# Kernel tuning notes

Measured on AMD Instinct MI355X. Metric: run time of the kernel, lower is better.

The kernel has to match this reference:

```python
import jax, jax.numpy as jnp
import numpy as np

EPS = 1e-5
CLUSTER_COUNT = 64
B, N, DV, DA = 128, 300, 1024, 128


def setup_inputs() -> dict:
    key = jax.random.key(0)
    k1, k2 = jax.random.split(key)
    video = jax.random.normal(k1, (B, N, DV), dtype=jnp.float32)
    audio = jax.random.normal(k2, (B, N, DA), dtype=jnp.float32)
    return {"video": video, "audio": audio}


def _select_indices(x_norm):
    """Greedy farthest-point (min |cosine|) selection for one batch. x_norm: [N, D]."""
    # indices starts as [0]; first appended index comes from sims of row 0
    best = jnp.abs(x_norm @ x_norm[0])          # [N]
    last = jnp.argmin(best)

    def step(carry, _):
        best, last = carry
        sims = jnp.abs(x_norm @ x_norm[last])   # [N]
        best = jnp.maximum(best, sims)
        new_last = jnp.argmin(best)
        return (best, new_last), new_last

    (_, _), rest = jax.lax.scan(step, (best, last), None, length=CLUSTER_COUNT - 2)
    idx = jnp.concatenate([jnp.array([0], dtype=last.dtype),
                           last[None], rest])  # [CLUSTER_COUNT]
    return jnp.sort(idx)


def reference(video, audio):
    # video: [B, N, DV], audio: [B, N, DA]
    norm = jnp.linalg.norm(video, axis=2) + EPS          # [B, N]
    video_normalized = video / norm[:, :, None]
    idx = jax.vmap(_select_indices)(video_normalized)     # [B, K], sorted
    v_sel = jnp.take_along_axis(video, idx[:, :, None], axis=1)  # [B, K, DV]
    a_sel = jnp.take_along_axis(audio, idx[:, :, None], axis=1)  # [B, K, DA]
    return v_sel, a_sel
```

## Files before the change

### kernel.cpp

```cpp
#include <hip/hip_runtime.h>
#include <math.h>


constexpr int BB = 128, NN = 300, DV = 1024, DA = 128, KK = 64;
constexpr int TRI = NN * (NN + 1) / 2;
constexpr int TB = 64;
constexpr int NTILES = 15;
constexpr int KC = 32;
constexpr int NCH = DV / KC;
constexpr int LDH = 36;

__device__ __constant__ int c_ib[NTILES] = {0,0,0,0,0, 1,1,1,1, 2,2,2, 3,3, 4};
__device__ __constant__ int c_jb[NTILES] = {0,1,2,3,4, 1,2,3,4, 2,3,4, 3,4, 4};

typedef _Float16 f16x8 __attribute__((ext_vector_type(8)));
typedef float    f32x4 __attribute__((ext_vector_type(4)));

union H4 { _Float16 h[4]; uint2 u; };
union F8 { uint2 u2[2]; f16x8 v; };

__device__ __forceinline__ int tri_base(int i) { return i * NN - (i * (i - 1)) / 2; }

__global__ __launch_bounds__(256) void kgram(const float* __restrict__ video,
                                             float* __restrict__ G) {
    const int bid  = blockIdx.x;
    const int swz  = (bid & 7) * 240 + (bid >> 3);
    const int batch = swz / 15;
    const int tile  = swz - batch * 15;
    const int i0 = c_ib[tile] * TB, j0 = c_jb[tile] * TB;
    const bool diag = (i0 == j0);
    const int tid = threadIdx.x;

    __shared__ _Float16 sH[2][4][TB][LDH];
    __shared__ float    s_part[256];
    __shared__ double   s_inv[2][TB];

    const float* vb = video + (size_t)batch * NN * DV;

    const int slab  = tid >> 7;
    const int lrow  = (tid >> 1) & 63;
    const int khalf = tid & 1;
    const int grow  = (slab ? j0 : i0) + lrow;
    const bool rok  = grow < NN;
    const bool stage_on = !(diag && slab == 1);
    const float4* srcb4 = (const float4*)(vb + (size_t)(rok ? grow : 0) * DV);
    const int qbase = khalf * 4;

    const int lane = tid & 63, w = tid >> 6;
    const int wr = w >> 1, wc = w & 1;
    const int g = lane >> 4, c16 = lane & 15;
    const int bplane = diag ? 0 : 2;

    f32x4 acc[2][2];
    #pragma unroll
    for (int fr = 0; fr < 2; ++fr)
        #pragma unroll
        for (int fc = 0; fc < 2; ++fc) acc[fr][fc] = (f32x4){0.f, 0.f, 0.f, 0.f};

    float ps = 0.f;
    float4 ld[4];
    const float4 z4 = make_float4(0.f, 0.f, 0.f, 0.f);

    auto stage_write = [&](int bf) {
        #pragma unroll
        for (int q = 0; q < 4; ++q) {
            float4 v = ld[q];
            ps = fmaf(v.x, v.x, fmaf(v.y, v.y, fmaf(v.z, v.z, fmaf(v.w, v.w, ps))));
            H4 hi, lo;
            _Float16 h0 = (_Float16)v.x, h1 = (_Float16)v.y,
                     h2 = (_Float16)v.z, h3 = (_Float16)v.w;
            hi.h[0] = h0; hi.h[1] = h1; hi.h[2] = h2; hi.h[3] = h3;
            lo.h[0] = (_Float16)(v.x - (float)h0);
            lo.h[1] = (_Float16)(v.y - (float)h1);
            lo.h[2] = (_Float16)(v.z - (float)h2);
            lo.h[3] = (_Float16)(v.w - (float)h3);
            const int p = khalf * 16 + 4 * q;
            *(uint2*)&sH[bf][slab * 2 + 0][lrow][p] = hi.u;
            *(uint2*)&sH[bf][slab * 2 + 1][lrow][p] = lo.u;
        }
    };

    if (stage_on) {
        #pragma unroll
        for (int q = 0; q < 4; ++q) ld[q] = rok ? srcb4[qbase + q] : z4;
        stage_write(0);
        #pragma unroll
        for (int q = 0; q < 4; ++q) ld[q] = rok ? srcb4[8 + qbase + q] : z4;
    }
    __syncthreads();

    for (int kc = 0; kc < NCH; ++kc) {
        const int cur = kc & 1, nxt = cur ^ 1;

        if (stage_on && kc < NCH - 1) stage_write(nxt);
        if (stage_on && kc < NCH - 2) {
            #pragma unroll
            for (int q = 0; q < 4; ++q)
                ld[q] = rok ? srcb4[(kc + 2) * 8 + qbase + q] : z4;
        }

        f16x8 Ah[2], Al[2], Bh[2], Bl[2];
        #pragma unroll
        for (int fr = 0; fr < 2; ++fr) {
            const int row = 32 * wr + 16 * fr + c16;
            F8 t;
            t.u2[0] = *(const uint2*)&sH[cur][0][row][4 * g];
            t.u2[1] = *(const uint2*)&sH[cur][0][row][16 + 4 * g];
            Ah[fr] = t.v;
            t.u2[0] = *(const uint2*)&sH[cur][1][row][4 * g];
            t.u2[1] = *(const uint2*)&sH[cur][1][row][16 + 4 * g];
            Al[fr] = t.v;
        }
        #pragma unroll
        for (int fc = 0; fc < 2; ++fc) {
            const int row = 32 * wc + 16 * fc + c16;
            F8 t;
            t.u2[0] = *(const uint2*)&sH[cur][bplane + 0][row][4 * g];
            t.u2[1] = *(const uint2*)&sH[cur][bplane + 0][row][16 + 4 * g];
            Bh[fc] = t.v;
            t.u2[0] = *(const uint2*)&sH[cur][bplane + 1][row][4 * g];
            t.u2[1] = *(const uint2*)&sH[cur][bplane + 1][row][16 + 4 * g];
            Bl[fc] = t.v;
        }
        #pragma unroll
        for (int fr = 0; fr < 2; ++fr)
            #pragma unroll
            for (int fc = 0; fc < 2; ++fc) {
                acc[fr][fc] = __builtin_amdgcn_mfma_f32_16x16x32_f16(Ah[fr], Bh[fc], acc[fr][fc], 0, 0, 0);
                acc[fr][fc] = __builtin_amdgcn_mfma_f32_16x16x32_f16(Ah[fr], Bl[fc], acc[fr][fc], 0, 0, 0);
                acc[fr][fc] = __builtin_amdgcn_mfma_f32_16x16x32_f16(Al[fr], Bh[fc], acc[fr][fc], 0, 0, 0);
            }

        __syncthreads();
    }

    s_part[tid] = ps;
    __syncthreads();
    if (tid < 128) {
        const int st = tid >> 6, r = tid & 63;
        const int src = (st && !diag) ? 128 + 2 * r : 2 * r;
        float ssum = s_part[src] + s_part[src + 1];
        s_inv[st][r] = 1.0 / (sqrt((double)ssum) + 1e-5);
    }
    __syncthreads();

    float* Gb = G + (size_t)batch * TRI;
    #pragma unroll
    for (int fr = 0; fr < 2; ++fr)
        #pragma unroll
        for (int fc = 0; fc < 2; ++fc)
            #pragma unroll
            for (int reg = 0; reg < 4; ++reg) {
                const int il = 32 * wr + 16 * fr + 4 * g + reg;
                const int jl = 32 * wc + 16 * fc + c16;
                const int i = i0 + il, j = j0 + jl;
                if (i <= j && j < NN)
                    Gb[tri_base(i) + (j - i)] =
                        (float)(fabs((double)acc[fr][fc][reg]) * s_inv[0][il] * s_inv[1][jl]);
            }
}

__device__ __forceinline__ void select_wave(const float* __restrict__ Gb,
                                            int lane, int* s_sorted) {
    float best[5];
    int myidx = 0;

    #pragma unroll
    for (int q = 0; q < 5; ++q) {
        int r = lane + 64 * q;
        best[q] = (r < NN) ? Gb[r] : 3.4e38f;
    }

    int last;
    {
        float v = INFINITY; int ri = 1 << 30;
        #pragma unroll
        for (int q = 0; q < 5; ++q)
            if (best[q] < v) { v = best[q]; ri = lane + 64 * q; }
        #pragma unroll
        for (int off = 32; off >= 1; off >>= 1) {
            float ov = __shfl_xor(v, off, 64); int oi = __shfl_xor(ri, off, 64);
            if (ov < v || (ov == v && oi < ri)) { v = ov; ri = oi; }
        }
        last = ri;
    }
    if (lane == 1) myidx = last;

    for (int t = 2; t < KK; ++t) {
        #pragma unroll
        for (int q = 0; q < 5; ++q) {
            int r = lane + 64 * q;
            if (r < NN) {
                int i = min(last, r), j = max(last, r);
                best[q] = fmaxf(best[q], Gb[tri_base(i) + (j - i)]);
            }
        }
        float v = INFINITY; int ri = 1 << 30;
        #pragma unroll
        for (int q = 0; q < 5; ++q)
            if (best[q] < v) { v = best[q]; ri = lane + 64 * q; }
        #pragma unroll
        for (int off = 32; off >= 1; off >>= 1) {
            float ov = __shfl_xor(v, off, 64); int oi = __shfl_xor(ri, off, 64);
            if (ov < v || (ov == v && oi < ri)) { v = ov; ri = oi; }
        }
        last = ri;
        if (lane == t) myidx = last;
    }

    int rank = 0;
    for (int j = 0; j < KK; ++j) {
        int oj = __shfl(myidx, j, 64);
        rank += (oj < myidx) || (oj == myidx && j < lane);
    }
    s_sorted[rank] = myidx;
}

__global__ __launch_bounds__(256) void kfused(const float* __restrict__ G,
                                              const float* __restrict__ video,
                                              const float* __restrict__ audio,
                                              float* __restrict__ out_v,
                                              float* __restrict__ out_a) {
    const int b = blockIdx.x, tid = threadIdx.x;
    __shared__ int s_sorted[KK];

    if (tid < 64)
        select_wave(G + (size_t)b * TRI, tid, s_sorted);
    __syncthreads();

    const float4* vb4 = (const float4*)(video + (size_t)b * NN * DV);
    float4* ov4 = (float4*)(out_v + (size_t)b * KK * DV);
    #pragma unroll 4
    for (int t = tid; t < KK * DV / 4; t += 256) {
        int k = t >> 8, c = t & 255;
        ov4[t] = vb4[s_sorted[k] * (DV / 4) + c];
    }
    const float4* ab4 = (const float4*)(audio + (size_t)b * NN * DA);
    float4* oa4 = (float4*)(out_a + (size_t)b * KK * DA);
    for (int t = tid; t < KK * DA / 4; t += 256) {
        int k = t >> 5, c = t & 31;
        oa4[t] = ab4[s_sorted[k] * (DA / 4) + c];
    }
}

__global__ __launch_bounds__(64) void kselect(const float* __restrict__ G,
                                              float* __restrict__ out_a) {
    __shared__ int s_sorted[KK];
    select_wave(G + (size_t)blockIdx.x * TRI, threadIdx.x, s_sorted);
    __syncthreads();
    ((int*)(out_a + (size_t)blockIdx.x * KK * DA))[threadIdx.x] = s_sorted[threadIdx.x];
}

__global__ __launch_bounds__(256) void kgather(const float* __restrict__ video,
                                               const float* __restrict__ audio,
                                               float* __restrict__ out_v,
                                               float* __restrict__ out_a) {
    int b = blockIdx.x, tid = threadIdx.x;
    __shared__ int s_idx[KK];
    const int* idxp = (const int*)(out_a + (size_t)b * KK * DA);
    if (tid < KK) s_idx[tid] = idxp[tid];
    __syncthreads();

    const float4* vb4 = (const float4*)(video + (size_t)b * NN * DV);
    float4* ov4 = (float4*)(out_v + (size_t)b * KK * DV);
    #pragma unroll 4
    for (int t = tid; t < KK * DV / 4; t += 256) {
        int k = t >> 8, c = t & 255;
        ov4[t] = vb4[s_idx[k] * (DV / 4) + c];
    }
    const float4* ab4 = (const float4*)(audio + (size_t)b * NN * DA);
    float4* oa4 = (float4*)(out_a + (size_t)b * KK * DA);
    for (int t = tid; t < KK * DA / 4; t += 256) {
        int k = t >> 5, c = t & 31;
        oa4[t] = ab4[s_idx[k] * (DA / 4) + c];
    }
}

extern "C" void kernel_launch(void* const* d_in, const int* in_sizes, int n_in,
                              void* d_out, int out_size, void* d_ws, size_t ws_size,
                              hipStream_t stream) {
    const float* video = (const float*)d_in[0];
    const float* audio = (const float*)d_in[1];
    float* out   = (float*)d_out;
    float* out_v = out;
    float* out_a = out + (size_t)BB * KK * DV;

    const size_t g_bytes = (size_t)BB * TRI * sizeof(float);
    if (ws_size >= g_bytes) {
        float* G = (float*)d_ws;
        kgram <<<NTILES * BB, 256, 0, stream>>>(video, G);
        kfused<<<BB, 256, 0, stream>>>(G, video, audio, out_v, out_a);
    } else {
        float* G = out;
        kgram  <<<NTILES * BB, 256, 0, stream>>>(video, G);
        kselect<<<BB, 64, 0, stream>>>(G, out_a);
        kgather<<<BB, 256, 0, stream>>>(video, audio, out_v, out_a);
    }
}
```

Baseline: 206.8 us.

## Pre-split video into fp16 hi/lo MFMA fragment layout before Gram kernel

Adds a prep kernel that converts each video row once into hi/lo fp16 pairs stored in the exact per-lane MFMA fragment order, and computes the inverse norms there. A new Gram kernel then loads fragments straight from global memory with no LDS staging or barriers. This removes the repeated fp32-to-fp16 split of the same rows across the five tiles that share them. The cost is an extra launch, a larger workspace, and an extra global write and read of the fragment buffer. The new path only runs when the workspace is big enough.

```diff
diff --git a/kernel.cpp b/kernel.cpp
--- a/kernel.cpp
+++ b/kernel.cpp
@@ -9,6 +9,14 @@
 constexpr int KC = 32;
 constexpr int NCH = DV / KC;
 constexpr int LDH = 36;
+constexpr int NRG = 20;
+
+constexpr size_t FRAG_U     = (size_t)NRG * NCH * 64;
+constexpr size_t FRAG_BYTES = FRAG_U * 16 * 2 * BB;
+constexpr size_t INV_OFF    = FRAG_BYTES;
+constexpr size_t INV_BYTES  = (size_t)BB * NN * 8;
+constexpr size_t G_OFF      = INV_OFF + INV_BYTES;
+constexpr size_t WS_NEED    = G_OFF + (size_t)BB * TRI * 4;
 
 __device__ __constant__ int c_ib[NTILES] = {0,0,0,0,0, 1,1,1,1, 2,2,2, 3,3, 4};
 __device__ __constant__ int c_jb[NTILES] = {0,1,2,3,4, 1,2,3,4, 2,3,4, 3,4, 4};
@@ -17,12 +25,128 @@
 typedef float    f32x4 __attribute__((ext_vector_type(4)));
 
 union H4 { _Float16 h[4]; uint2 u; };
+union H8 { _Float16 h[8]; f16x8 v; };
 union F8 { uint2 u2[2]; f16x8 v; };
 
 __device__ __forceinline__ int tri_base(int i) { return i * NN - (i * (i - 1)) / 2; }
 
-__global__ __launch_bounds__(256) void kgram(const float* __restrict__ video,
-                                             float* __restrict__ G) {
+__global__ __launch_bounds__(256) void kprep(const float* __restrict__ video,
+                                             _Float16* __restrict__ F,
+                                             double* __restrict__ invn) {
+    const int rg = blockIdx.x, b = blockIdx.y;
+    const int tid = threadIdx.x, w = tid >> 6, lane = tid & 63;
+    const int g = lane >> 4, c16 = lane & 15;
+    const int row = rg * 16 + c16;
+    const bool rv = row < NN;
+    const float* vr = video + (size_t)b * NN * DV + (size_t)(rv ? row : 0) * DV;
+    const float4 z4 = make_float4(0.f, 0.f, 0.f, 0.f);
+
+    f16x8* Fv = (f16x8*)F;
+    const size_t baseHi = ((size_t)(b * 2 + 0) * NRG + rg) * (NCH * 64) + lane;
+    const size_t baseLo = ((size_t)(b * 2 + 1) * NRG + rg) * (NCH * 64) + lane;
+
+    float ps = 0.f;
+    for (int kc = w; kc < NCH; kc += 4) {
+        const int k0 = kc * KC;
+        float4 a = rv ? *(const float4*)(vr + k0 + 4 * g) : z4;
+        float4 c = rv ? *(const float4*)(vr + k0 + 16 + 4 * g) : z4;
+        ps = fmaf(a.x, a.x, fmaf(a.y, a.y, fmaf(a.z, a.z, fmaf(a.w, a.w, ps))));
+        ps = fmaf(c.x, c.x, fmaf(c.y, c.y, fmaf(c.z, c.z, fmaf(c.w, c.w, ps))));
+        float s[8] = {a.x, a.y, a.z, a.w, c.x, c.y, c.z, c.w};
+        H8 hi, lo;
+        #pragma unroll
+        for (int e = 0; e < 8; ++e) {
+            _Float16 h = (_Float16)s[e];
+            hi.h[e] = h;
+            lo.h[e] = (_Float16)(s[e] - (float)h);
+        }
+        Fv[baseHi + kc * 64] = hi.v;
+        Fv[baseLo + kc * 64] = lo.v;
+    }
+
+    ps += __shfl_xor(ps, 16, 64);
+    ps += __shfl_xor(ps, 32, 64);
+    __shared__ float sr[4][16];
+    if (lane < 16) sr[w][c16] = ps;
+    __syncthreads();
+    if (tid < 16) {
+        const int rr = rg * 16 + tid;
+        if (rr < NN) {
+            double sum = (double)sr[0][tid] + (double)sr[1][tid]
+                       + (double)sr[2][tid] + (double)sr[3][tid];
+            invn[b * NN + rr] = 1.0 / (sqrt(sum) + 1e-5);
+        }
+    }
+}
+
+__global__ __launch_bounds__(256) void kgram2(const _Float16* __restrict__ F,
+                                              const double* __restrict__ invn,
+                                              float* __restrict__ G) {
+    const int bid  = blockIdx.x;
+    const int swz  = (bid & 7) * 240 + (bid >> 3);
+    const int batch = swz / 15;
+    const int tile  = swz - batch * 15;
+    const int i0 = c_ib[tile] * TB, j0 = c_jb[tile] * TB;
+    const int tid = threadIdx.x, lane = tid & 63, w = tid >> 6;
+    const int wr = w >> 1, wc = w & 1;
+    const int g = lane >> 4, c16 = lane & 15;
+
+    const f16x8* Fv = (const f16x8*)F;
+    const f16x8 *pAh[2], *pAl[2], *pBh[2], *pBl[2];
+    #pragma unroll
+    for (int fr = 0; fr < 2; ++fr) {
+        const int rgA = (i0 >> 4) + 2 * wr + fr;
+        const int rgB = (j0 >> 4) + 2 * wc + fr;
+        pAh[fr] = Fv + ((size_t)(batch * 2 + 0) * NRG + rgA) * (NCH * 64) + lane;
+        pAl[fr] = Fv + ((size_t)(batch * 2 + 1) * NRG + rgA) * (NCH * 64) + lane;
+        pBh[fr] = Fv + ((size_t)(batch * 2 + 0) * NRG + rgB) * (NCH * 64) + lane;
+        pBl[fr] = Fv + ((size_t)(batch * 2 + 1) * NRG + rgB) * (NCH * 64) + lane;
+    }
+
+    f32x4 acc[2][2];
+    #pragma unroll
+    for (int fr = 0; fr < 2; ++fr)
+        #pragma unroll
+        for (int fc = 0; fc < 2; ++fc) acc[fr][fc] = (f32x4){0.f, 0.f, 0.f, 0.f};
+
+    #pragma unroll 2
+    for (int kc = 0; kc < NCH; ++kc) {
+        const int o = kc * 64;
+        f16x8 Ah[2], Al[2], Bh[2], Bl[2];
+        #pragma unroll
+        for (int fr = 0; fr < 2; ++fr) {
+            Ah[fr] = pAh[fr][o]; Al[fr] = pAl[fr][o];
+            Bh[fr] = pBh[fr][o]; Bl[fr] = pBl[fr][o];
+        }
+        #pragma unroll
+        for (int fr = 0; fr < 2; ++fr)
+            #pragma unroll
+            for (int fc = 0; fc < 2; ++fc) {
+                acc[fr][fc] = __builtin_amdgcn_mfma_f32_16x16x32_f16(Ah[fr], Bh[fc], acc[fr][fc], 0, 0, 0);
+                acc[fr][fc] = __builtin_amdgcn_mfma_f32_16x16x32_f16(Ah[fr], Bl[fc], acc[fr][fc], 0, 0, 0);
+                acc[fr][fc] = __builtin_amdgcn_mfma_f32_16x16x32_f16(Al[fr], Bh[fc], acc[fr][fc], 0, 0, 0);
+            }
+    }
+
+    const double* invb = invn + batch * NN;
+    float* Gb = G + (size_t)batch * TRI;
+    #pragma unroll
+    for (int fr = 0; fr < 2; ++fr)
+        #pragma unroll
+        for (int fc = 0; fc < 2; ++fc)
+            #pragma unroll
+            for (int reg = 0; reg < 4; ++reg) {
+                const int il = 32 * wr + 16 * fr + 4 * g + reg;
+                const int jl = 32 * wc + 16 * fc + c16;
+                const int i = i0 + il, j = j0 + jl;
+                if (i <= j && j < NN)
+                    Gb[tri_base(i) + (j - i)] =
+                        (float)(fabs((double)acc[fr][fc][reg]) * invb[i] * invb[j]);
+            }
+}
+
+__global__ __launch_bounds__(256) void kgram_lds(const float* __restrict__ video,
+                                                 float* __restrict__ G) {
     const int bid  = blockIdx.x;
     const int swz  = (bid & 7) * 240 + (bid >> 3);
     const int batch = swz / 15;
@@ -91,7 +215,6 @@
 
     for (int kc = 0; kc < NCH; ++kc) {
         const int cur = kc & 1, nxt = cur ^ 1;
-
         if (stage_on && kc < NCH - 1) stage_write(nxt);
         if (stage_on && kc < NCH - 2) {
             #pragma unroll
@@ -130,7 +253,6 @@
                 acc[fr][fc] = __builtin_amdgcn_mfma_f32_16x16x32_f16(Ah[fr], Bl[fc], acc[fr][fc], 0, 0, 0);
                 acc[fr][fc] = __builtin_amdgcn_mfma_f32_16x16x32_f16(Al[fr], Bh[fc], acc[fr][fc], 0, 0, 0);
             }
-
         __syncthreads();
     }
 
@@ -286,14 +408,22 @@
     float* out_a = out + (size_t)BB * KK * DV;
 
     const size_t g_bytes = (size_t)BB * TRI * sizeof(float);
-    if (ws_size >= g_bytes) {
+
+    if (ws_size >= WS_NEED) {
+        _Float16* F  = (_Float16*)d_ws;
+        double* invn = (double*)((char*)d_ws + INV_OFF);
+        float* G     = (float*)((char*)d_ws + G_OFF);
+        kprep <<<dim3(NRG, BB), 256, 0, stream>>>(video, F, invn);
+        kgram2<<<NTILES * BB, 256, 0, stream>>>(F, invn, G);
+        kfused<<<BB, 256, 0, stream>>>(G, video, audio, out_v, out_a);
+    } else if (ws_size >= g_bytes) {
         float* G = (float*)d_ws;
-        kgram <<<NTILES * BB, 256, 0, stream>>>(video, G);
-        kfused<<<BB, 256, 0, stream>>>(G, video, audio, out_v, out_a);
+        kgram_lds<<<NTILES * BB, 256, 0, stream>>>(video, G);
+        kfused   <<<BB, 256, 0, stream>>>(G, video, audio, out_v, out_a);
     } else {
         float* G = out;
-        kgram  <<<NTILES * BB, 256, 0, stream>>>(video, G);
-        kselect<<<BB, 64, 0, stream>>>(G, out_a);
-        kgather<<<BB, 256, 0, stream>>>(video, audio, out_v, out_a);
-    }
-}
+        kgram_lds<<<NTILES * BB, 256, 0, stream>>>(video, G);
+        kselect  <<<BB, 64, 0, stream>>>(G, out_a);
+        kgather  <<<BB, 256, 0, stream>>>(video, audio, out_v, out_a);
+    }
+}
```

Result: slower. 272.8 us (+31.9%).

## Use 128x128 gram tiles and a padded square gram matrix for selection

Applied to the files above, without the earlier changes.

Adds a new gram kernel that uses 512-thread blocks computing 128x128 tiles, six per batch instead of fifteen 64x64 tiles. This gives more operand reuse per LDS load and fewer redundant video reads. The kernel writes the gram matrix as a full symmetric square with a padded stride of 304, so the selection loop reads a contiguous row instead of the triangular layout. The cost is a larger workspace, twice as many global stores, and higher register pressure from the larger accumulator. The older triangular path remains as a fallback when the workspace is too small.

```diff
diff --git a/kernel.cpp b/kernel.cpp
--- a/kernel.cpp
+++ b/kernel.cpp
@@ -4,12 +4,20 @@
 
 constexpr int BB = 128, NN = 300, DV = 1024, DA = 128, KK = 64;
 constexpr int TRI = NN * (NN + 1) / 2;
-constexpr int TB = 64;
-constexpr int NTILES = 15;
 constexpr int KC = 32;
 constexpr int NCH = DV / KC;
 constexpr int LDH = 36;
 
+constexpr int GS = 304;
+constexpr int GBATCH = NN * GS;
+constexpr size_t SQ_NEED = (size_t)BB * GBATCH * 4;
+
+constexpr int NT2 = 6;
+__device__ __constant__ int t2_ib[NT2] = {0,0,0,1,1,2};
+__device__ __constant__ int t2_jb[NT2] = {0,1,2,1,2,2};
+
+constexpr int NTILES = 15;
+constexpr int TB = 64;
 __device__ __constant__ int c_ib[NTILES] = {0,0,0,0,0, 1,1,1,1, 2,2,2, 3,3, 4};
 __device__ __constant__ int c_jb[NTILES] = {0,1,2,3,4, 1,2,3,4, 2,3,4, 3,4, 4};
 
@@ -21,25 +29,26 @@
 
 __device__ __forceinline__ int tri_base(int i) { return i * NN - (i * (i - 1)) / 2; }
 
-__global__ __launch_bounds__(256) void kgram(const float* __restrict__ video,
-                                             float* __restrict__ G) {
+__global__ __launch_bounds__(512, 4) void kgram3(const float* __restrict__ video,
+                                                 float* __restrict__ G) {
     const int bid  = blockIdx.x;
-    const int swz  = (bid & 7) * 240 + (bid >> 3);
-    const int batch = swz / 15;
-    const int tile  = swz - batch * 15;
-    const int i0 = c_ib[tile] * TB, j0 = c_jb[tile] * TB;
+    const int swz  = (bid & 7) * 96 + (bid >> 3);
+    const int batch = swz / NT2;
+    const int tile  = swz - batch * NT2;
+    const int i0 = t2_ib[tile] * 128, j0 = t2_jb[tile] * 128;
     const bool diag = (i0 == j0);
     const int tid = threadIdx.x;
 
-    __shared__ _Float16 sH[2][4][TB][LDH];
-    __shared__ float    s_part[256];
-    __shared__ double   s_inv[2][TB];
+    __shared__ _Float16 sH[2][4][128][LDH];
+    __shared__ float    s_part[512];
+    __shared__ double   s_inv[2][128];
 
     const float* vb = video + (size_t)batch * NN * DV;
 
-    const int slab  = tid >> 7;
-    const int lrow  = (tid >> 1) & 63;
-    const int khalf = tid & 1;
+    const int slab  = tid >> 8;
+    const int st    = tid & 255;
+    const int lrow  = st >> 1;
+    const int khalf = st & 1;
     const int grow  = (slab ? j0 : i0) + lrow;
     const bool rok  = grow < NN;
     const bool stage_on = !(diag && slab == 1);
@@ -47,13 +56,13 @@
     const int qbase = khalf * 4;
 
     const int lane = tid & 63, w = tid >> 6;
-    const int wr = w >> 1, wc = w & 1;
+    const int wr2 = w >> 2, wc2 = w & 3;
     const int g = lane >> 4, c16 = lane & 15;
     const int bplane = diag ? 0 : 2;
 
-    f32x4 acc[2][2];
+    f32x4 acc[4][2];
     #pragma unroll
-    for (int fr = 0; fr < 2; ++fr)
+    for (int fr = 0; fr < 4; ++fr)
         #pragma unroll
         for (int fc = 0; fc < 2; ++fc) acc[fr][fc] = (f32x4){0.f, 0.f, 0.f, 0.f};
 
@@ -91,7 +100,146 @@
 
     for (int kc = 0; kc < NCH; ++kc) {
         const int cur = kc & 1, nxt = cur ^ 1;
-
+        if (stage_on && kc < NCH - 1) stage_write(nxt);
+        if (stage_on && kc < NCH - 2) {
+            #pragma unroll
+            for (int q = 0; q < 4; ++q)
+                ld[q] = rok ? srcb4[(kc + 2) * 8 + qbase + q] : z4;
+        }
+
+        f16x8 Ah[4], Al[4], Bh[2], Bl[2];
+        #pragma unroll
+        for (int fr = 0; fr < 4; ++fr) {
+            const int row = 64 * wr2 + 16 * fr + c16;
+            F8 t;
+            t.u2[0] = *(const uint2*)&sH[cur][0][row][4 * g];
+            t.u2[1] = *(const uint2*)&sH[cur][0][row][16 + 4 * g];
+            Ah[fr] = t.v;
+            t.u2[0] = *(const uint2*)&sH[cur][1][row][4 * g];
+            t.u2[1] = *(const uint2*)&sH[cur][1][row][16 + 4 * g];
+            Al[fr] = t.v;
+        }
+        #pragma unroll
+        for (int fc = 0; fc < 2; ++fc) {
+            const int row = 32 * wc2 + 16 * fc + c16;
+            F8 t;
+            t.u2[0] = *(const uint2*)&sH[cur][bplane + 0][row][4 * g];
+            t.u2[1] = *(const uint2*)&sH[cur][bplane + 0][row][16 + 4 * g];
+            Bh[fc] = t.v;
+            t.u2[0] = *(const uint2*)&sH[cur][bplane + 1][row][4 * g];
+            t.u2[1] = *(const uint2*)&sH[cur][bplane + 1][row][16 + 4 * g];
+            Bl[fc] = t.v;
+        }
+        #pragma unroll
+        for (int fr = 0; fr < 4; ++fr)
+            #pragma unroll
+            for (int fc = 0; fc < 2; ++fc) {
+                acc[fr][fc] = __builtin_amdgcn_mfma_f32_16x16x32_f16(Ah[fr], Bh[fc], acc[fr][fc], 0, 0, 0);
+                acc[fr][fc] = __builtin_amdgcn_mfma_f32_16x16x32_f16(Ah[fr], Bl[fc], acc[fr][fc], 0, 0, 0);
+                acc[fr][fc] = __builtin_amdgcn_mfma_f32_16x16x32_f16(Al[fr], Bh[fc], acc[fr][fc], 0, 0, 0);
+            }
+        __syncthreads();
+    }
+
+    s_part[tid] = ps;
+    __syncthreads();
+    if (tid < 256) {
+        const int sl = tid >> 7, r = tid & 127;
+        const int src = (sl && !diag) ? 256 + 2 * r : 2 * r;
+        float ssum = s_part[src] + s_part[src + 1];
+        s_inv[sl][r] = 1.0 / (sqrt((double)ssum) + 1e-5);
+    }
+    __syncthreads();
+
+    float* Gb = G + (size_t)batch * GBATCH;
+    #pragma unroll
+    for (int fr = 0; fr < 4; ++fr)
+        #pragma unroll
+        for (int fc = 0; fc < 2; ++fc)
+            #pragma unroll
+            for (int reg = 0; reg < 4; ++reg) {
+                const int il = 64 * wr2 + 16 * fr + 4 * g + reg;
+                const int jl = 32 * wc2 + 16 * fc + c16;
+                const int i = i0 + il, j = j0 + jl;
+                if (i <= j && j < NN) {
+                    float val = (float)(fabs((double)acc[fr][fc][reg]) *
+                                        s_inv[0][il] * s_inv[1][jl]);
+                    Gb[i * GS + j] = val;
+                    Gb[j * GS + i] = val;
+                }
+            }
+}
+
+__global__ __launch_bounds__(256) void kgram_lds(const float* __restrict__ video,
+                                                 float* __restrict__ G) {
+    const int bid  = blockIdx.x;
+    const int swz  = (bid & 7) * 240 + (bid >> 3);
+    const int batch = swz / 15;
+    const int tile  = swz - batch * 15;
+    const int i0 = c_ib[tile] * TB, j0 = c_jb[tile] * TB;
+    const bool diag = (i0 == j0);
+    const int tid = threadIdx.x;
+
+    __shared__ _Float16 sH[2][4][TB][LDH];
+    __shared__ float    s_part[256];
+    __shared__ double   s_inv[2][TB];
+
+    const float* vb = video + (size_t)batch * NN * DV;
+
+    const int slab  = tid >> 7;
+    const int lrow  = (tid >> 1) & 63;
+    const int khalf = tid & 1;
+    const int grow  = (slab ? j0 : i0) + lrow;
+    const bool rok  = grow < NN;
+    const bool stage_on = !(diag && slab == 1);
+    const float4* srcb4 = (const float4*)(vb + (size_t)(rok ? grow : 0) * DV);
+    const int qbase = khalf * 4;
+
+    const int lane = tid & 63, w = tid >> 6;
+    const int wr = w >> 1, wc = w & 1;
+    const int g = lane >> 4, c16 = lane & 15;
+    const int bplane = diag ? 0 : 2;
+
+    f32x4 acc[2][2];
+    #pragma unroll
+    for (int fr = 0; fr < 2; ++fr)
+        #pragma unroll
+        for (int fc = 0; fc < 2; ++fc) acc[fr][fc] = (f32x4){0.f, 0.f, 0.f, 0.f};
+
+    float ps = 0.f;
+    float4 ld[4];
+    const float4 z4 = make_float4(0.f, 0.f, 0.f, 0.f);
+
+    auto stage_write = [&](int bf) {
+        #pragma unroll
+        for (int q = 0; q < 4; ++q) {
+            float4 v = ld[q];
+            ps = fmaf(v.x, v.x, fmaf(v.y, v.y, fmaf(v.z, v.z, fmaf(v.w, v.w, ps))));
+            H4 hi, lo;
+            _Float16 h0 = (_Float16)v.x, h1 = (_Float16)v.y,
+                     h2 = (_Float16)v.z, h3 = (_Float16)v.w;
+            hi.h[0] = h0; hi.h[1] = h1; hi.h[2] = h2; hi.h[3] = h3;
+            lo.h[0] = (_Float16)(v.x - (float)h0);
+            lo.h[1] = (_Float16)(v.y - (float)h1);
+            lo.h[2] = (_Float16)(v.z - (float)h2);
+            lo.h[3] = (_Float16)(v.w - (float)h3);
+            const int p = khalf * 16 + 4 * q;
+            *(uint2*)&sH[bf][slab * 2 + 0][lrow][p] = hi.u;
+            *(uint2*)&sH[bf][slab * 2 + 1][lrow][p] = lo.u;
+        }
+    };
+
+    if (stage_on) {
+        #pragma unroll
+        for (int q = 0; q < 4; ++q) ld[q] = rok ? srcb4[qbase + q] : z4;
+        stage_write(0);
+        #pragma unroll
+        for (int q = 0; q < 4; ++q) ld[q] = rok ? srcb4[8 + qbase + q] : z4;
+    }
+    __syncthreads();
+
+    for (int kc = 0; kc < NCH; ++kc) {
+        const int cur = kc & 1, nxt = cur ^ 1;
         if (stage_on && kc < NCH - 1) stage_write(nxt);
         if (stage_on && kc < NCH - 2) {
             #pragma unroll
@@ -130,17 +278,16 @@
                 acc[fr][fc] = __builtin_amdgcn_mfma_f32_16x16x32_f16(Ah[fr], Bl[fc], acc[fr][fc], 0, 0, 0);
                 acc[fr][fc] = __builtin_amdgcn_mfma_f32_16x16x32_f16(Al[fr], Bh[fc], acc[fr][fc], 0, 0, 0);
             }
-
         __syncthreads();
     }
 
     s_part[tid] = ps;
     __syncthreads();
     if (tid < 128) {
-        const int st = tid >> 6, r = tid & 63;
-        const int src = (st && !diag) ? 128 + 2 * r : 2 * r;
+        const int sl = tid >> 6, r = tid & 63;
+        const int src = (sl && !diag) ? 128 + 2 * r : 2 * r;
         float ssum = s_part[src] + s_part[src + 1];
-        s_inv[st][r] = 1.0 / (sqrt((double)ssum) + 1e-5);
+        s_inv[sl][r] = 1.0 / (sqrt((double)ssum) + 1e-5);
     }
     __syncthreads();
 
@@ -160,8 +307,62 @@
             }
 }
 
-__device__ __forceinline__ void select_wave(const float* __restrict__ Gb,
-                                            int lane, int* s_sorted) {
+__device__ __forceinline__ void select_wave_sq(const float* __restrict__ Gb,
+                                               int lane, int* s_sorted) {
+    float best[5];
+    int myidx = 0;
+
+    #pragma unroll
+    for (int q = 0; q < 5; ++q) {
+        int r = lane + 64 * q;
+        best[q] = (r < NN) ? Gb[r] : 3.4e38f;
+    }
+
+    int last;
+    {
+        float v = INFINITY; int ri = 1 << 30;
+        #pragma unroll
+        for (int q = 0; q < 5; ++q)
+            if (best[q] < v) { v = best[q]; ri = lane + 64 * q; }
+        #pragma unroll
+        for (int off = 32; off >= 1; off >>= 1) {
+            float ov = __shfl_xor(v, off, 64); int oi = __shfl_xor(ri, off, 64);
+            if (ov < v || (ov == v && oi < ri)) { v = ov; ri = oi; }
+        }
+        last = ri;
+    }
+    if (lane == 1) myidx = last;
+
+    for (int t = 2; t < KK; ++t) {
+        const float* row = Gb + last * GS;
+        #pragma unroll
+        for (int q = 0; q < 5; ++q) {
+            int r = lane + 64 * q;
+            if (r < NN) best[q] = fmaxf(best[q], row[r]);
+        }
+        float v = INFINITY; int ri = 1 << 30;
+        #pragma unroll
+        for (int q = 0; q < 5; ++q)
+            if (best[q] < v) { v = best[q]; ri = lane + 64 * q; }
+        #pragma unroll
+        for (int off = 32; off >= 1; off >>= 1) {
+            float ov = __shfl_xor(v, off, 64); int oi = __shfl_xor(ri, off, 64);
+            if (ov < v || (ov == v && oi < ri)) { v = ov; ri = oi; }
+        }
+        last = ri;
+        if (lane == t) myidx = last;
+    }
+
+    int rank = 0;
+    for (int j = 0; j < KK; ++j) {
+        int oj = __shfl(myidx, j, 64);
+        rank += (oj < myidx) || (oj == myidx && j < lane);
+    }
+    s_sorted[rank] = myidx;
+}
+
+__device__ __forceinline__ void select_wave_tri(const float* __restrict__ Gb,
+                                                int lane, int* s_sorted) {
     float best[5];
     int myidx = 0;
 
@@ -216,16 +417,16 @@
     s_sorted[rank] = myidx;
 }
 
-__global__ __launch_bounds__(256) void kfused(const float* __restrict__ G,
-                                              const float* __restrict__ video,
-                                              const float* __restrict__ audio,
-                                              float* __restrict__ out_v,
-                                              float* __restrict__ out_a) {
+__global__ __launch_bounds__(256) void kfused_sq(const float* __restrict__ G,
+                                                 const float* __restrict__ video,
+                                                 const float* __restrict__ audio,
+                                                 float* __restrict__ out_v,
+                                                 float* __restrict__ out_a) {
     const int b = blockIdx.x, tid = threadIdx.x;
     __shared__ int s_sorted[KK];
 
     if (tid < 64)
-        select_wave(G + (size_t)b * TRI, tid, s_sorted);
+        select_wave_sq(G + (size_t)b * GBATCH, tid, s_sorted);
     __syncthreads();
 
     const float4* vb4 = (const float4*)(video + (size_t)b * NN * DV);
@@ -243,10 +444,37 @@
     }
 }
 
+__global__ __launch_bounds__(256) void kfused_tri(const float* __restrict__ G,
+                                                  const float* __restrict__ video,
+                                                  const float* __restrict__ audio,
+                                                  float* __restrict__ out_v,
+                                                  float* __restrict__ out_a) {
+    const int b = blockIdx.x, tid = threadIdx.x;
+    __shared__ int s_sorted[KK];
+
+    if (tid < 64)
+        select_wave_tri(G + (size_t)b * TRI, tid, s_sorted);
+    __syncthreads();
+
+    const float4* vb4 = (const float4*)(video + (size_t)b * NN * DV);
+    float4* ov4 = (float4*)(out_v + (size_t)b * KK * DV);
+    #pragma unroll 4
+    for (int t = tid; t < KK * DV / 4; t += 256) {
+        int k = t >> 8, c = t & 255;
+        ov4[t] = vb4[s_sorted[k] * (DV / 4) + c];
+    }
+    const float4* ab4 = (const float4*)(audio + (size_t)b * NN * DA);
+    float4* oa4 = (float4*)(out_a + (size_t)b * KK * DA);
+    for (int t = tid; t < KK * DA / 4; t += 256) {
+        int k = t >> 5, c = t & 31;
+        oa4[t] = ab4[s_sorted[k] * (DA / 4) + c];
+    }
+}
+
 __global__ __launch_bounds__(64) void kselect(const float* __restrict__ G,
                                               float* __restrict__ out_a) {
     __shared__ int s_sorted[KK];
-    select_wave(G + (size_t)blockIdx.x * TRI, threadIdx.x, s_sorted);
+    select_wave_tri(G + (size_t)blockIdx.x * TRI, threadIdx.x, s_sorted);
     __syncthreads();
     ((int*)(out_a + (size_t)blockIdx.x * KK * DA))[threadIdx.x] = s_sorted[threadIdx.x];
 }
@@ -285,15 +513,20 @@
     float* out_v = out;
     float* out_a = out + (size_t)BB * KK * DV;
 
-    const size_t g_bytes = (size_t)BB * TRI * sizeof(float);
-    if (ws_size >= g_bytes) {
+    const size_t tri_bytes = (size_t)BB * TRI * sizeof(float);
+
+    if (ws_size >= SQ_NEED) {
         float* G = (float*)d_ws;
-        kgram <<<NTILES * BB, 256, 0, stream>>>(video, G);
-        kfused<<<BB, 256, 0, stream>>>(G, video, audio, out_v, out_a);
+        kgram3   <<<NT2 * BB, 512, 0, stream>>>(video, G);
+        kfused_sq<<<BB, 256, 0, stream>>>(G, video, audio, out_v, out_a);
+    } else if (ws_size >= tri_bytes) {
+        float* G = (float*)d_ws;
+        kgram_lds <<<NTILES * BB, 256, 0, stream>>>(video, G);
+        kfused_tri<<<BB, 256, 0, stream>>>(G, video, audio, out_v, out_a);
     } else {
         float* G = out;
-        kgram  <<<NTILES * BB, 256, 0, stream>>>(video, G);
-        kselect<<<BB, 64, 0, stream>>>(G, out_a);
-        kgather<<<BB, 256, 0, stream>>>(video, audio, out_v, out_a);
-    }
-}
+        kgram_lds<<<NTILES * BB, 256, 0, stream>>>(video, G);
+        kselect  <<<BB, 64, 0, stream>>>(G, out_a);
+        kgather  <<<BB, 256, 0, stream>>>(video, audio, out_v, out_a);
+    }
+}
```

Measured after the change: 214.6 us. +3.7%, slower.

## Use 512-thread gram blocks, pad per-batch triangle, and prefetch G in select kernel

Applied to the files above, without the earlier changes.

The gram kernel now runs 8 waves per block, so each wave computes a 32x16 sub-tile and each thread stages two float4 loads per chunk instead of four. This is meant to raise parallelism and hide latency. The per-batch triangle stride is padded to a 16-byte aligned size so the fused kernel can sweep the whole batch's G slab with float4 loads first. That sweep warms the cache before the serial greedy selection wave reads it. The cost is extra global reads and a dummy reduction, and each loaded B fragment is now reused by fewer MFMAs.

```diff
diff --git a/kernel.cpp b/kernel.cpp
--- a/kernel.cpp
+++ b/kernel.cpp
@@ -3,7 +3,8 @@
 
 
 constexpr int BB = 128, NN = 300, DV = 1024, DA = 128, KK = 64;
-constexpr int TRI = NN * (NN + 1) / 2;
+constexpr int TRI  = NN * (NN + 1) / 2;
+constexpr int TRIP = 45152;
 constexpr int TB = 64;
 constexpr int NTILES = 15;
 constexpr int KC = 32;
@@ -21,8 +22,8 @@
 
 __device__ __forceinline__ int tri_base(int i) { return i * NN - (i * (i - 1)) / 2; }
 
-__global__ __launch_bounds__(256) void kgram(const float* __restrict__ video,
-                                             float* __restrict__ G) {
+__global__ __launch_bounds__(512) void kgram512(const float* __restrict__ video,
+                                                float* __restrict__ G) {
     const int bid  = blockIdx.x;
     const int swz  = (bid & 7) * 240 + (bid >> 3);
     const int batch = swz / 15;
@@ -32,38 +33,37 @@
     const int tid = threadIdx.x;
 
     __shared__ _Float16 sH[2][4][TB][LDH];
-    __shared__ float    s_part[256];
+    __shared__ float    s_part[512];
     __shared__ double   s_inv[2][TB];
 
     const float* vb = video + (size_t)batch * NN * DV;
 
-    const int slab  = tid >> 7;
-    const int lrow  = (tid >> 1) & 63;
-    const int khalf = tid & 1;
-    const int grow  = (slab ? j0 : i0) + lrow;
-    const bool rok  = grow < NN;
+    const int slab = tid >> 8;
+    const int st   = tid & 255;
+    const int lrow = st >> 2;
+    const int part = st & 3;
+    const int grow = (slab ? j0 : i0) + lrow;
+    const bool rok = grow < NN;
     const bool stage_on = !(diag && slab == 1);
     const float4* srcb4 = (const float4*)(vb + (size_t)(rok ? grow : 0) * DV);
-    const int qbase = khalf * 4;
+    const int qbase = part * 2;
 
     const int lane = tid & 63, w = tid >> 6;
-    const int wr = w >> 1, wc = w & 1;
+    const int wr3 = w >> 2, wc3 = w & 3;
     const int g = lane >> 4, c16 = lane & 15;
     const int bplane = diag ? 0 : 2;
 
-    f32x4 acc[2][2];
-    #pragma unroll
-    for (int fr = 0; fr < 2; ++fr)
-        #pragma unroll
-        for (int fc = 0; fc < 2; ++fc) acc[fr][fc] = (f32x4){0.f, 0.f, 0.f, 0.f};
+    f32x4 acc[2];
+    acc[0] = (f32x4){0.f, 0.f, 0.f, 0.f};
+    acc[1] = (f32x4){0.f, 0.f, 0.f, 0.f};
 
     float ps = 0.f;
-    float4 ld[4];
+    float4 ld[2];
     const float4 z4 = make_float4(0.f, 0.f, 0.f, 0.f);
 
     auto stage_write = [&](int bf) {
         #pragma unroll
-        for (int q = 0; q < 4; ++q) {
+        for (int q = 0; q < 2; ++q) {
             float4 v = ld[q];
             ps = fmaf(v.x, v.x, fmaf(v.y, v.y, fmaf(v.z, v.z, fmaf(v.w, v.w, ps))));
             H4 hi, lo;
@@ -74,18 +74,18 @@
             lo.h[1] = (_Float16)(v.y - (float)h1);
             lo.h[2] = (_Float16)(v.z - (float)h2);
             lo.h[3] = (_Float16)(v.w - (float)h3);
-            const int p = khalf * 16 + 4 * q;
+            const int p = part * 8 + 4 * q;
             *(uint2*)&sH[bf][slab * 2 + 0][lrow][p] = hi.u;
             *(uint2*)&sH[bf][slab * 2 + 1][lrow][p] = lo.u;
         }
     };
 
     if (stage_on) {
-        #pragma unroll
-        for (int q = 0; q < 4; ++q) ld[q] = rok ? srcb4[qbase + q] : z4;
+        ld[0] = rok ? srcb4[qbase] : z4;
+        ld[1] = rok ? srcb4[qbase + 1] : z4;
         stage_write(0);
-        #pragma unroll
-        for (int q = 0; q < 4; ++q) ld[q] = rok ? srcb4[8 + qbase + q] : z4;
+        ld[0] = rok ? srcb4[8 + qbase] : z4;
+        ld[1] = rok ? srcb4[8 + qbase + 1] : z4;
     }
     __syncthreads();
 
@@ -94,15 +94,14 @@
 
         if (stage_on && kc < NCH - 1) stage_write(nxt);
         if (stage_on && kc < NCH - 2) {
-            #pragma unroll
-            for (int q = 0; q < 4; ++q)
-                ld[q] = rok ? srcb4[(kc + 2) * 8 + qbase + q] : z4;
-        }
-
-        f16x8 Ah[2], Al[2], Bh[2], Bl[2];
+            ld[0] = rok ? srcb4[(kc + 2) * 8 + qbase] : z4;
+            ld[1] = rok ? srcb4[(kc + 2) * 8 + qbase + 1] : z4;
+        }
+
+        f16x8 Ah[2], Al[2], Bh, Bl;
         #pragma unroll
         for (int fr = 0; fr < 2; ++fr) {
-            const int row = 32 * wr + 16 * fr + c16;
+            const int row = 32 * wr3 + 16 * fr + c16;
             F8 t;
             t.u2[0] = *(const uint2*)&sH[cur][0][row][4 * g];
             t.u2[1] = *(const uint2*)&sH[cur][0][row][16 + 4 * g];
@@ -111,25 +110,22 @@
             t.u2[1] = *(const uint2*)&sH[cur][1][row][16 + 4 * g];
             Al[fr] = t.v;
         }
-        #pragma unroll
-        for (int fc = 0; fc < 2; ++fc) {
-            const int row = 32 * wc + 16 * fc + c16;
+        {
+            const int row = 16 * wc3 + c16;
             F8 t;
             t.u2[0] = *(const uint2*)&sH[cur][bplane + 0][row][4 * g];
             t.u2[1] = *(const uint2*)&sH[cur][bplane + 0][row][16 + 4 * g];
-            Bh[fc] = t.v;
+            Bh = t.v;
             t.u2[0] = *(const uint2*)&sH[cur][bplane + 1][row][4 * g];
             t.u2[1] = *(const uint2*)&sH[cur][bplane + 1][row][16 + 4 * g];
-            Bl[fc] = t.v;
-        }
-        #pragma unroll
-        for (int fr = 0; fr < 2; ++fr)
-            #pragma unroll
-            for (int fc = 0; fc < 2; ++fc) {
-                acc[fr][fc] = __builtin_amdgcn_mfma_f32_16x16x32_f16(Ah[fr], Bh[fc], acc[fr][fc], 0, 0, 0);
-                acc[fr][fc] = __builtin_amdgcn_mfma_f32_16x16x32_f16(Ah[fr], Bl[fc], acc[fr][fc], 0, 0, 0);
-                acc[fr][fc] = __builtin_amdgcn_mfma_f32_16x16x32_f16(Al[fr], Bh[fc], acc[fr][fc], 0, 0, 0);
-            }
+            Bl = t.v;
+        }
+        #pragma unroll
+        for (int fr = 0; fr < 2; ++fr) {
+            acc[fr] = __builtin_amdgcn_mfma_f32_16x16x32_f16(Ah[fr], Bh, acc[fr], 0, 0, 0);
+            acc[fr] = __builtin_amdgcn_mfma_f32_16x16x32_f16(Ah[fr], Bl, acc[fr], 0, 0, 0);
+            acc[fr] = __builtin_amdgcn_mfma_f32_16x16x32_f16(Al[fr], Bh, acc[fr], 0, 0, 0);
+        }
 
         __syncthreads();
     }
@@ -137,31 +133,29 @@
     s_part[tid] = ps;
     __syncthreads();
     if (tid < 128) {
-        const int st = tid >> 6, r = tid & 63;
-        const int src = (st && !diag) ? 128 + 2 * r : 2 * r;
-        float ssum = s_part[src] + s_part[src + 1];
-        s_inv[st][r] = 1.0 / (sqrt((double)ssum) + 1e-5);
-    }
-    __syncthreads();
-
-    float* Gb = G + (size_t)batch * TRI;
+        const int sl = tid >> 6, r = tid & 63;
+        const int src = (sl && !diag) ? 256 + 4 * r : 4 * r;
+        float ssum = s_part[src] + s_part[src + 1] + s_part[src + 2] + s_part[src + 3];
+        s_inv[sl][r] = 1.0 / (sqrt((double)ssum) + 1e-5);
+    }
+    __syncthreads();
+
+    float* Gb = G + (size_t)batch * TRIP;
     #pragma unroll
     for (int fr = 0; fr < 2; ++fr)
         #pragma unroll
-        for (int fc = 0; fc < 2; ++fc)
-            #pragma unroll
-            for (int reg = 0; reg < 4; ++reg) {
-                const int il = 32 * wr + 16 * fr + 4 * g + reg;
-                const int jl = 32 * wc + 16 * fc + c16;
-                const int i = i0 + il, j = j0 + jl;
-                if (i <= j && j < NN)
-                    Gb[tri_base(i) + (j - i)] =
-                        (float)(fabs((double)acc[fr][fc][reg]) * s_inv[0][il] * s_inv[1][jl]);
-            }
-}
-
-__device__ __forceinline__ void select_wave(const float* __restrict__ Gb,
-                                            int lane, int* s_sorted) {
+        for (int reg = 0; reg < 4; ++reg) {
+            const int il = 32 * wr3 + 16 * fr + 4 * g + reg;
+            const int jl = 16 * wc3 + c16;
+            const int i = i0 + il, j = j0 + jl;
+            if (i <= j && j < NN)
+                Gb[tri_base(i) + (j - i)] =
+                    (float)(fabs((double)acc[fr][reg]) * s_inv[0][il] * s_inv[1][jl]);
+        }
+}
+
+__device__ __forceinline__ void select_wave_tri(const float* __restrict__ Gb,
+                                                int lane, int* s_sorted) {
     float best[5];
     int myidx = 0;
 
@@ -224,8 +218,21 @@
     const int b = blockIdx.x, tid = threadIdx.x;
     __shared__ int s_sorted[KK];
 
+    const float* Gb = G + (size_t)b * TRIP;
+
+    {
+        const float4* G4 = (const float4*)Gb;
+        float s = 0.f;
+        for (int t = tid; t < TRIP / 4; t += 256) {
+            float4 v = G4[t];
+            s += v.x + v.y + v.z + v.w;
+        }
+        asm volatile("" :: "v"(s));
+    }
+    __syncthreads();
+
     if (tid < 64)
-        select_wave(G + (size_t)b * TRI, tid, s_sorted);
+        select_wave_tri(Gb, tid, s_sorted);
     __syncthreads();
 
     const float4* vb4 = (const float4*)(video + (size_t)b * NN * DV);
@@ -246,7 +253,7 @@
 __global__ __launch_bounds__(64) void kselect(const float* __restrict__ G,
                                               float* __restrict__ out_a) {
     __shared__ int s_sorted[KK];
-    select_wave(G + (size_t)blockIdx.x * TRI, threadIdx.x, s_sorted);
+    select_wave_tri(G + (size_t)blockIdx.x * TRIP, threadIdx.x, s_sorted);
     __syncthreads();
     ((int*)(out_a + (size_t)blockIdx.x * KK * DA))[threadIdx.x] = s_sorted[threadIdx.x];
 }
@@ -285,15 +292,16 @@
     float* out_v = out;
     float* out_a = out + (size_t)BB * KK * DV;
 
-    const size_t g_bytes = (size_t)BB * TRI * sizeof(float);
+    const size_t g_bytes = (size_t)BB * TRIP * sizeof(float);
+
     if (ws_size >= g_bytes) {
         float* G = (float*)d_ws;
-        kgram <<<NTILES * BB, 256, 0, stream>>>(video, G);
-        kfused<<<BB, 256, 0, stream>>>(G, video, audio, out_v, out_a);
+        kgram512<<<NTILES * BB, 512, 0, stream>>>(video, G);
+        kfused  <<<BB, 256, 0, stream>>>(G, video, audio, out_v, out_a);
     } else {
         float* G = out;
-        kgram  <<<NTILES * BB, 256, 0, stream>>>(video, G);
-        kselect<<<BB, 64, 0, stream>>>(G, out_a);
-        kgather<<<BB, 256, 0, stream>>>(video, audio, out_v, out_a);
-    }
-}
+        kgram512<<<NTILES * BB, 512, 0, stream>>>(video, G);
+        kselect <<<BB, 64, 0, stream>>>(G, out_a);
+        kgather <<<BB, 256, 0, stream>>>(video, audio, out_v, out_a);
+    }
+}
```

Measured after the change: 479.8 us. 132% more time.
